# Kernel optimization log

Measured on AMD Instinct MI355X. Metric: run time of the kernel, lower is better.

Reference implementation:

```python
import jax, jax.numpy as jnp
import numpy as np

CLIP_LEN = 16
IN_CH = 64  # math.ceil(256 // 4 / 4) * 4
BN_EPS = 1e-5


def setup_inputs() -> dict:
    key = jax.random.key(0)
    ks = jax.random.split(key, 7)
    x = jax.random.normal(ks[0], (128, 256, 56, 56), jnp.float32)
    bn_gamma = 1.0 + 0.1 * jax.random.normal(ks[1], (IN_CH,), jnp.float32)
    bn_beta = 0.1 * jax.random.normal(ks[2], (IN_CH,), jnp.float32)
    bn_mean = 0.1 * jax.random.normal(ks[3], (IN_CH,), jnp.float32)
    bn_var = jax.random.uniform(ks[4], (IN_CH,), jnp.float32, minval=0.5, maxval=1.5)
    # groups=2 Conv3d: out=2, in_per_group=IN_CH//2, kernel 3x3x3
    conv_w = 0.02 * jax.random.normal(ks[5], (2, IN_CH // 2, 3, 3, 3), jnp.float32)
    conv_b = 0.02 * jax.random.normal(ks[6], (2,), jnp.float32)
    return dict(x=x, bn_gamma=bn_gamma, bn_beta=bn_beta, bn_mean=bn_mean,
                bn_var=bn_var, conv_w=conv_w, conv_b=conv_b)


def _gsm(x5, bn_gamma, bn_beta, bn_mean, bn_var, conv_w, conv_b):
    # x5: [n, c, t, h, w] with c == IN_CH
    n, c, t, h, w = x5.shape
    scale = bn_gamma * jax.lax.rsqrt(bn_var + BN_EPS)          # [c]
    shift = bn_beta - bn_mean * scale                          # [c]
    x_act = jax.nn.relu(x5 * scale[None, :, None, None, None]
                        + shift[None, :, None, None, None])
    gate = jnp.tanh(
        jax.lax.conv_general_dilated(
            x_act, conv_w, window_strides=(1, 1, 1), padding='SAME',
            dimension_numbers=('NCDHW', 'OIDHW', 'NCDHW'),
            feature_group_count=2)
        + conv_b[None, :, None, None, None])                   # [n,2,t,h,w]
    half = c // 2

    def gated_shift(xg, g, left):
        y = g * xg                                             # gated part
        r = xg - y                                             # residual part
        if left:
            y_sh = jnp.concatenate([y[:, :, 1:], jnp.zeros_like(y[:, :, :1])], axis=2)
        else:
            y_sh = jnp.concatenate([jnp.zeros_like(y[:, :, :1]), y[:, :, :-1]], axis=2)
        out = y_sh + r
        # channel regroup: [n,2,c/4,t,h,w] -> permute -> [n,c/2,t,h,w]
        return out.reshape(n, 2, half // 2, t, h, w).transpose(0, 2, 1, 3, 4, 5).reshape(n, half, t, h, w)

    y1 = gated_shift(x5[:, :half], gate[:, 0:1], left=True)
    y2 = gated_shift(x5[:, half:], gate[:, 1:2], left=False)
    return jnp.concatenate([y1, y2], axis=1)


def reference(x, bn_gamma, bn_beta, bn_mean, bn_var, conv_w, conv_b):
    nt, c, h, w = x.shape
    n = nt // CLIP_LEN
    # [nt, IN_CH, h, w] -> [n, IN_CH, T, h, w]
    xs = x[:, :IN_CH].reshape(n, CLIP_LEN, IN_CH, h, w).transpose(0, 2, 1, 3, 4)
    y = _gsm(xs, bn_gamma, bn_beta, bn_mean, bn_var, conv_w, conv_b)
    y = y.transpose(0, 2, 1, 3, 4).reshape(nt, IN_CH, h, w)
    # remaining channels pass through unchanged; net wrapper is identity
    return jnp.concatenate([y, x[:, IN_CH:]], axis=1)
```

## Files before the change

kernel.cpp:

```cpp
#include <hip/hip_runtime.h>
#include <math.h>

namespace {
constexpr int kT = 16;
constexpr int kH = 56;
constexpr int kW = 56;
constexpr int kCAll = 256;
constexpr int kPlane = kH * kW;
constexpr int kPlane4 = kPlane / 4;
}


__global__ __launch_bounds__(256, 2)
void gate_conv_kernel(const float* __restrict__ x,
                      const float* __restrict__ gamma,
                      const float* __restrict__ beta,
                      const float* __restrict__ mean,
                      const float* __restrict__ var,
                      const float* __restrict__ cw,
                      const float* __restrict__ cb,
                      float* __restrict__ gate) {
  __shared__ float4 smb[4 * 510];

  const int bid = blockIdx.x;
  const int stripe = bid & 1;
  const int g = (bid >> 1) & 1;
  const int t = (bid >> 2) & 15;
  const int n = bid >> 6;
  const int h0 = stripe * 28;
  const int tid = threadIdx.x;
  const int wid = tid >> 6;
  const int lane = tid & 63;
  const int r = lane >> 1;
  const int h = lane & 1;
  const int wbase = wid * 510;

  for (int i = lane; i < 510; i += 64)
    smb[wbase + i] = make_float4(0.f, 0.f, 0.f, 0.f);

  int rr_u[7], fb_u[7], go_u[7];
  bool val_u[7];
  #pragma unroll
  for (int u = 0; u < 7; ++u) {
    const int j = lane + u * 64;
    bool v = (j < 420);
    int rr = 0, fb = 0, go = 0;
    if (v) {
      rr = j / 14;
      fb = j - rr * 14;
      const int gr = h0 + rr - 1;
      v = ((unsigned)gr < (unsigned)kH);
      if (v) go = gr * 14 + fb;
    }
    rr_u[u] = rr; fb_u[u] = fb; go_u[u] = go; val_u[u] = v;
  }

  float acc[28];
  #pragma unroll
  for (int p = 0; p < 28; ++p) acc[p] = 0.f;

  auto loadS = [&](int s, float4 (&pf)[7]) {
    const int il = s / 3;
    const int kd = s - il * 3;
    const int tt = t + kd - 1;
    const int ch = g * 32 + wid * 8 + il;
    if (tt >= 0 && tt < kT) {
      const float4* src4 =
          (const float4*)x + ((size_t)(n * kT + tt) * kCAll + ch) * kPlane4;
      #pragma unroll
      for (int u = 0; u < 7; ++u)
        pf[u] = val_u[u] ? src4[go_u[u]] : make_float4(0.f, 0.f, 0.f, 0.f);
    } else {
      #pragma unroll
      for (int u = 0; u < 7; ++u) pf[u] = make_float4(0.f, 0.f, 0.f, 0.f);
    }
  };

  auto stageS = [&](int s, const float4 (&pf)[7]) {
    const int il = s / 3;
    const int kd = s - il * 3;
    const int tt = t + kd - 1;
    if (tt < 0 || tt >= kT) return;
    const int ch = g * 32 + wid * 8 + il;
    const float sc = gamma[ch] * rsqrtf(var[ch] + 1e-5f);
    const float sh = beta[ch] - mean[ch] * sc;
    #pragma unroll
    for (int u = 0; u < 7; ++u) {
      if (val_u[u]) {
        float4 a = pf[u];
        a.x = fmaxf(0.f, fmaf(a.x, sc, sh));
        a.y = fmaxf(0.f, fmaf(a.y, sc, sh));
        a.z = fmaxf(0.f, fmaf(a.z, sc, sh));
        a.w = fmaxf(0.f, fmaf(a.w, sc, sh));
        smb[wbase + rr_u[u] * 17 + fb_u[u] + 1] = a;
      }
    }
  };

  auto computeS = [&](int s) {
    const int il = s / 3;
    const int kd = s - il * 3;
    const int tt = t + kd - 1;
    if (tt < 0 || tt >= kT) return;
    if (r >= 28) return;
    const int ch = g * 32 + wid * 8 + il;
    const float* wbp = cw + ch * 27 + kd * 9;
    float wk[9];
    #pragma unroll
    for (int j = 0; j < 9; ++j) wk[j] = wbp[j];
    #pragma unroll
    for (int kh = 0; kh < 3; ++kh) {
      const int base = wbase + (r + kh) * 17 + 7 * h;
      float f[36];
      #pragma unroll
      for (int jj = 0; jj < 9; ++jj) {
        const float4 B = smb[base + jj];
        f[4 * jj + 0] = B.x; f[4 * jj + 1] = B.y;
        f[4 * jj + 2] = B.z; f[4 * jj + 3] = B.w;
      }
      const float w0 = wk[kh * 3 + 0];
      const float w1 = wk[kh * 3 + 1];
      const float w2 = wk[kh * 3 + 2];
      #pragma unroll
      for (int p = 0; p < 28; ++p)
        acc[p] = fmaf(f[p + 3], w0,
                 fmaf(f[p + 4], w1, fmaf(f[p + 5], w2, acc[p])));
    }
  };

  float4 A[7], B[7];
  loadS(0, A);
  for (int s2 = 0; s2 < 24; s2 += 2) {
    if (s2 + 1 < 24) loadS(s2 + 1, B);
    stageS(s2, A);
    computeS(s2);
    if (s2 + 2 < 24) loadS(s2 + 2, A);
    if (s2 + 1 < 24) { stageS(s2 + 1, B); computeS(s2 + 1); }
  }

  __syncthreads();
  float* smf = (float*)smb;
  if (r < 28) {
    const int q0 = r * 56 + h * 28;
    #pragma unroll
    for (int p = 0; p < 28; ++p) smf[wid * 1568 + q0 + p] = acc[p];
  }
  __syncthreads();
  const float bias = cb[g];
  float* gp = gate + ((size_t)(n * 2 + g) * kT + t) * kPlane + h0 * kW;
  for (int q = tid; q < 1568; q += 256) {
    float s = smf[q] + smf[1568 + q] + smf[2 * 1568 + q] + smf[3 * 1568 + q];
    gp[q] = tanhf(s + bias);
  }
}

__global__ __launch_bounds__(256)
void copy_gate_slice_kernel(float4* __restrict__ o4) {
  const int j = blockIdx.x * 256 + threadIdx.x;
  if (j >= 3 * kPlane4) return;
  const int q = j / kPlane4;
  const int rr = j - q * kPlane4;
  const int pidx = (q == 0) ? 239 : (q == 1 ? 254 : 255);
  const size_t G1 = (size_t)127 * kCAll * kPlane4;
  const size_t H = ((size_t)126 * kCAll + 64) * kPlane4;
  o4[H + j] = o4[G1 + (size_t)pidx * kPlane4 + rr];
}

__global__ __launch_bounds__(256)
void shift_main_kernel(const float4* __restrict__ x4,
                       const float4* __restrict__ g4,
                       float4* __restrict__ o4) {
  const size_t total = (size_t)127 * kCAll * kPlane4;
  const size_t idx = (size_t)blockIdx.x * 256 + threadIdx.x;
  if (idx >= total) return;

  const int p = (int)(idx % kPlane4);
  const size_t rest = idx / kPlane4;
  const int c = (int)(rest % kCAll);
  const int f = (int)(rest / kCAll);

  if (c >= 64) {
    if (f == 126 && c <= 66) return;
    o4[idx] = x4[idx];
    return;
  }

  const int n = f >> 4;
  const int t = f & 15;
  const int half = c >> 5;
  const int k = c & 31;
  const int m = ((k & 1) << 4) + (k >> 1);
  const int src_ch = half * 32 + m;

  const size_t xcur = ((size_t)f * kCAll + src_ch) * kPlane4 + p;
  const size_t gbase = (size_t)(n * 2 + half) * kT * kPlane4 + p;

  const float4 xc = x4[xcur];
  const float4 gc = g4[gbase + (size_t)t * kPlane4];
  float4 y = make_float4(0.f, 0.f, 0.f, 0.f);
  if (half == 0) {
    if (t < kT - 1) {
      const float4 xn = x4[xcur + (size_t)kCAll * kPlane4];
      const float4 gn = g4[gbase + (size_t)(t + 1) * kPlane4];
      y.x = gn.x * xn.x; y.y = gn.y * xn.y; y.z = gn.z * xn.z; y.w = gn.w * xn.w;
    }
  } else {
    if (t > 0) {
      const float4 xp = x4[xcur - (size_t)kCAll * kPlane4];
      const float4 gp = g4[gbase + (size_t)(t - 1) * kPlane4];
      y.x = gp.x * xp.x; y.y = gp.y * xp.y; y.z = gp.z * xp.z; y.w = gp.w * xp.w;
    }
  }
  float4 res;
  res.x = y.x + (xc.x - gc.x * xc.x);
  res.y = y.y + (xc.y - gc.y * xc.y);
  res.z = y.z + (xc.z - gc.z * xc.z);
  res.w = y.w + (xc.w - gc.w * xc.w);
  o4[idx] = res;
}

__global__ __launch_bounds__(256)
void last_frame_kernel(const float4* __restrict__ x4,
                       float4* o4) {
  const int idx = blockIdx.x * 256 + threadIdx.x;
  if (idx >= kCAll * kPlane4) return;
  const size_t F127 = (size_t)127 * kCAll * kPlane4;
  const int p = idx % kPlane4;
  const int c = idx / kPlane4;
  if (c >= 64) { o4[F127 + idx] = x4[F127 + idx]; return; }

  const size_t H = ((size_t)126 * kCAll + 64) * kPlane4;
  const int half = c >> 5;
  const int k = c & 31;
  const int m = ((k & 1) << 4) + (k >> 1);
  const int src_ch = half * 32 + m;

  const float4 xc = x4[F127 + (size_t)src_ch * kPlane4 + p];
  float4 gc;
  float4 y = make_float4(0.f, 0.f, 0.f, 0.f);
  if (half == 0) {
    gc = o4[H + 0 * kPlane4 + p];
  } else {
    gc = o4[H + 2 * kPlane4 + p];
    const float4 gp = o4[H + 1 * kPlane4 + p];
    const float4 xp = x4[((size_t)126 * kCAll + src_ch) * kPlane4 + p];
    y.x = gp.x * xp.x; y.y = gp.y * xp.y; y.z = gp.z * xp.z; y.w = gp.w * xp.w;
  }
  float4 res;
  res.x = y.x + (xc.x - gc.x * xc.x);
  res.y = y.y + (xc.y - gc.y * xc.y);
  res.z = y.z + (xc.z - gc.z * xc.z);
  res.w = y.w + (xc.w - gc.w * xc.w);
  o4[F127 + idx] = res;
}

__global__ __launch_bounds__(256)
void fix_hole_kernel(const float4* __restrict__ x4, float4* __restrict__ o4) {
  const int j = blockIdx.x * 256 + threadIdx.x;
  if (j >= 3 * kPlane4) return;
  const size_t H = ((size_t)126 * kCAll + 64) * kPlane4;
  o4[H + j] = x4[H + j];
}

extern "C" void kernel_launch(void* const* d_in, const int* in_sizes, int n_in,
                              void* d_out, int out_size, void* d_ws, size_t ws_size,
                              hipStream_t stream) {
  const float* x     = (const float*)d_in[0];
  const float* gamma = (const float*)d_in[1];
  const float* beta  = (const float*)d_in[2];
  const float* mean  = (const float*)d_in[3];
  const float* var   = (const float*)d_in[4];
  const float* cw    = (const float*)d_in[5];
  const float* cb    = (const float*)d_in[6];
  float* out = (float*)d_out;

  float* gate = out + (size_t)127 * kCAll * kPlane;

  gate_conv_kernel<<<512, 256, 0, stream>>>(x, gamma, beta, mean, var, cw, cb, gate);
  copy_gate_slice_kernel<<<10, 256, 0, stream>>>((float4*)out);

  const size_t total4 = (size_t)127 * kCAll * kPlane4;
  shift_main_kernel<<<(unsigned)((total4 + 255) / 256), 256, 0, stream>>>(
      (const float4*)x, (const float4*)gate, (float4*)out);

  last_frame_kernel<<<(kCAll * kPlane4 + 255) / 256, 256, 0, stream>>>(
      (const float4*)x, (float4*)out);
  fix_hole_kernel<<<10, 256, 0, stream>>>((const float4*)x, (float4*)out);
}
```

Measured before the change: 224.9 us.

## Fuse passthrough channel copy into gate conv kernel and use workspace for gate

Extra blocks are appended to the gate convolution launch to copy the 192 passthrough channels, so that bandwidth-bound copy overlaps with the compute-bound conv. The shift kernel now processes only the first 64 channels. When a large enough workspace is provided, the gate is stored there instead of in the output's last frame, which removes the slice-copy, last-frame and hole-fix kernels. This relies on the workspace being available and couples two unrelated workloads in one launch, which may disturb conv occupancy and scheduling.

```diff
diff --git a/kernel.cpp b/kernel.cpp
--- a/kernel.cpp
+++ b/kernel.cpp
@@ -8,19 +8,37 @@
 constexpr int kCAll = 256;
 constexpr int kPlane = kH * kW;
 constexpr int kPlane4 = kPlane / 4;
+constexpr size_t kGateBytes = (size_t)256 * kPlane * sizeof(float);
 }
 
 
 __global__ __launch_bounds__(256, 2)
-void gate_conv_kernel(const float* __restrict__ x,
-                      const float* __restrict__ gamma,
-                      const float* __restrict__ beta,
-                      const float* __restrict__ mean,
-                      const float* __restrict__ var,
-                      const float* __restrict__ cw,
-                      const float* __restrict__ cb,
-                      float* __restrict__ gate) {
+void fused_conv_copy_kernel(const float* __restrict__ x,
+                            const float* __restrict__ gamma,
+                            const float* __restrict__ beta,
+                            const float* __restrict__ mean,
+                            const float* __restrict__ var,
+                            const float* __restrict__ cw,
+                            const float* __restrict__ cb,
+                            float* __restrict__ gate,
+                            const float4* __restrict__ x4,
+                            float4* __restrict__ o4,
+                            int nf_copy, int skip_hole) {
   __shared__ float4 smb[4 * 510];
+
+  if (blockIdx.x >= 512) {
+    const size_t j = (size_t)(blockIdx.x - 512) * 256 + threadIdx.x;
+    const size_t total = (size_t)nf_copy * 192 * kPlane4;
+    if (j >= total) return;
+    const int f = (int)(j / (192 * kPlane4));
+    const int rem = (int)(j - (size_t)f * 192 * kPlane4);
+    const int c = 64 + rem / kPlane4;
+    const int p = rem - (c - 64) * kPlane4;
+    if (skip_hole && f == 126 && c <= 66) return;
+    const size_t idx = ((size_t)f * kCAll + c) * kPlane4 + p;
+    o4[idx] = x4[idx];
+    return;
+  }
 
   const int bid = blockIdx.x;
   const int stripe = bid & 1;
@@ -167,23 +185,17 @@
 }
 
 __global__ __launch_bounds__(256)
-void shift_main_kernel(const float4* __restrict__ x4,
-                       const float4* __restrict__ g4,
-                       float4* __restrict__ o4) {
-  const size_t total = (size_t)127 * kCAll * kPlane4;
-  const size_t idx = (size_t)blockIdx.x * 256 + threadIdx.x;
-  if (idx >= total) return;
-
-  const int p = (int)(idx % kPlane4);
-  const size_t rest = idx / kPlane4;
-  const int c = (int)(rest % kCAll);
-  const int f = (int)(rest / kCAll);
-
-  if (c >= 64) {
-    if (f == 126 && c <= 66) return;
-    o4[idx] = x4[idx];
-    return;
-  }
+void shift_c64_kernel(const float4* __restrict__ x4,
+                      const float4* __restrict__ g4,
+                      float4* __restrict__ o4, int nf) {
+  const size_t total = (size_t)nf * 64 * kPlane4;
+  const size_t j = (size_t)blockIdx.x * 256 + threadIdx.x;
+  if (j >= total) return;
+
+  const int p = (int)(j % kPlane4);
+  const size_t rest = j / kPlane4;
+  const int c = (int)(rest % 64);
+  const int f = (int)(rest / 64);
 
   const int n = f >> 4;
   const int t = f & 15;
@@ -211,12 +223,13 @@
       y.x = gp.x * xp.x; y.y = gp.y * xp.y; y.z = gp.z * xp.z; y.w = gp.w * xp.w;
     }
   }
+  const size_t oidx = ((size_t)f * kCAll + c) * kPlane4 + p;
   float4 res;
   res.x = y.x + (xc.x - gc.x * xc.x);
   res.y = y.y + (xc.y - gc.y * xc.y);
   res.z = y.z + (xc.z - gc.z * xc.z);
   res.w = y.w + (xc.w - gc.w * xc.w);
-  o4[idx] = res;
+  o4[oidx] = res;
 }
 
 __global__ __launch_bounds__(256)
@@ -274,16 +287,27 @@
   const float* cb    = (const float*)d_in[6];
   float* out = (float*)d_out;
 
-  float* gate = out + (size_t)127 * kCAll * kPlane;
-
-  gate_conv_kernel<<<512, 256, 0, stream>>>(x, gamma, beta, mean, var, cw, cb, gate);
-  copy_gate_slice_kernel<<<10, 256, 0, stream>>>((float4*)out);
-
-  const size_t total4 = (size_t)127 * kCAll * kPlane4;
-  shift_main_kernel<<<(unsigned)((total4 + 255) / 256), 256, 0, stream>>>(
-      (const float4*)x, (const float4*)gate, (float4*)out);
-
-  last_frame_kernel<<<(kCAll * kPlane4 + 255) / 256, 256, 0, stream>>>(
-      (const float4*)x, (float4*)out);
-  fix_hole_kernel<<<10, 256, 0, stream>>>((const float4*)x, (float4*)out);
-}
+  const bool use_ws = (d_ws != nullptr) && (ws_size >= kGateBytes);
+  float* gate = use_ws ? (float*)d_ws : out + (size_t)127 * kCAll * kPlane;
+  const int nf = use_ws ? 128 : 127;
+  const int skip_hole = use_ws ? 0 : 1;
+
+  const int copy_total = nf * 192 * kPlane4;
+  const int copy_blocks = (copy_total + 255) / 256;
+  fused_conv_copy_kernel<<<512 + copy_blocks, 256, 0, stream>>>(
+      x, gamma, beta, mean, var, cw, cb, gate,
+      (const float4*)x, (float4*)out, nf, skip_hole);
+
+  if (!use_ws)
+    copy_gate_slice_kernel<<<10, 256, 0, stream>>>((float4*)out);
+
+  const int shift_total = nf * 64 * kPlane4;
+  shift_c64_kernel<<<(shift_total + 255) / 256, 256, 0, stream>>>(
+      (const float4*)x, (const float4*)gate, (float4*)out, nf);
+
+  if (!use_ws) {
+    last_frame_kernel<<<(kCAll * kPlane4 + 255) / 256, 256, 0, stream>>>(
+        (const float4*)x, (float4*)out);
+    fix_hole_kernel<<<10, 256, 0, stream>>>((const float4*)x, (float4*)out);
+  }
+}
```

Result: slower. 290.2 us (+29.0%).
